# Optimization experiments

Measured on AMD Instinct MI355X. Metric: run time of the kernel, lower is better.

The kernel has to match this reference:

```python
import jax, jax.numpy as jnp
import numpy as np

EMBED_DIM = 1024
NUM_HEADS = 16
HEAD_DIM = EMBED_DIM // NUM_HEADS
ROPE_BASE = 10000.0


def setup_inputs() -> dict:
    key = jax.random.key(0)
    ks = jax.random.split(key, 5)
    B, S, E = 4, 2048, EMBED_DIM
    hidden = jax.random.normal(ks[0], (B, S, E), dtype=jnp.float32)
    sc_in = 1.0 / np.sqrt(E)
    qkv_w = jax.random.normal(ks[1], (3 * E, E), dtype=jnp.float32) * sc_in
    qkv_b = jnp.zeros((3 * E,), dtype=jnp.float32)
    proj_w = jax.random.normal(ks[2], (E, E), dtype=jnp.float32) * sc_in
    proj_b = jnp.zeros((E,), dtype=jnp.float32)
    return {"hidden": hidden, "qkv_w": qkv_w, "qkv_b": qkv_b,
            "proj_w": proj_w, "proj_b": proj_b}


def _rope_cos_sin(position_ids, head_dim, base):
    # position_ids: [B, S] int; returns cos/sin of shape [B, 1, S, head_dim]
    inv_freq = 1.0 / (base ** (jnp.arange(0, head_dim, 2, dtype=jnp.float32) / head_dim))
    freqs = position_ids.astype(jnp.float32)[..., None] * inv_freq  # [B,S,hd/2]
    emb = jnp.concatenate([freqs, freqs], axis=-1)                  # [B,S,hd]
    return jnp.cos(emb)[:, None], jnp.sin(emb)[:, None]


def _rotate_half(x):
    x1, x2 = jnp.split(x, 2, axis=-1)
    return jnp.concatenate([-x2, x1], axis=-1)


def reference(hidden, qkv_w, qkv_b, proj_w, proj_b):
    B, S, E = hidden.shape
    H, hd = NUM_HEADS, HEAD_DIM
    qkv = hidden @ qkv_w.T + qkv_b                    # [B,S,3E]
    qkv = qkv.reshape(B, S, 3, H, hd).transpose(2, 0, 3, 1, 4)  # [3,B,H,S,hd]
    q, k, v = qkv[0], qkv[1], qkv[2]
    pos = jnp.broadcast_to(jnp.arange(S)[None, :], (B, S))
    cos, sin = _rope_cos_sin(pos, hd, ROPE_BASE)      # [B,1,S,hd]
    q = q * cos + _rotate_half(q) * sin
    k = k * cos + _rotate_half(k) * sin
    scale = 1.0 / jnp.sqrt(jnp.float32(hd))
    scores = jnp.einsum("bhsd,bhtd->bhst", q, k) * scale
    attn = jax.nn.softmax(scores, axis=-1)
    out = jnp.einsum("bhst,bhtd->bhsd", attn, v)      # [B,H,S,hd]
    out = out.transpose(0, 2, 1, 3).reshape(B, S, E)
    return out @ proj_w.T + proj_b
```

## Files before the change

kernel.cpp:

```cpp
#include <hip/hip_runtime.h>
#include <cstdint>
#include <cstddef>

typedef _Float16 f16;
typedef __attribute__((ext_vector_type(4))) float f32x4;
typedef __attribute__((ext_vector_type(8))) _Float16 f16x8;
typedef __attribute__((ext_vector_type(4))) _Float16 f16x4;

#define S_SEQ 2048
#define E_DIM 1024

#define OFF_HID   0ull
#define OFF_QKVW  8388608ull
#define OFF_PROJW 11534336ull
#define OFF_Q     12582912ull
#define OFF_K     20971520ull
#define OFF_VT    29360128ull
#define OFF_AO    37748736ull

__device__ __forceinline__ void async_copy16(const void* g, void* l) {
  __builtin_amdgcn_global_load_lds(
      (const __attribute__((address_space(1))) unsigned int*)g,
      (__attribute__((address_space(3))) unsigned int*)l, 16, 0, 0);
}

__device__ __forceinline__ float fast_exp2(float x) {
#if __has_builtin(__builtin_amdgcn_exp2f)
  return __builtin_amdgcn_exp2f(x);
#else
  return __expf(x * 0.6931471805599453f);
#endif
}

__global__ __launch_bounds__(256) void cvt_kernel(const float* __restrict__ hid,
                                                  const float* __restrict__ qw,
                                                  const float* __restrict__ pw,
                                                  f16* __restrict__ ws) {
  long i = (long)blockIdx.x * 256 + threadIdx.x;
  const float* src;
  f16* dst;
  long idx;
  if (i < 2097152L) { src = hid; dst = ws + OFF_HID;  idx = i; }
  else if (i < 2883584L) { src = qw; dst = ws + OFF_QKVW; idx = i - 2097152L; }
  else { src = pw; dst = ws + OFF_PROJW; idx = i - 2883584L; }
  float4 v = *(const float4*)(src + idx * 4);
  f16x4 o = { (f16)v.x, (f16)v.y, (f16)v.z, (f16)v.w };
  *(f16x4*)(dst + idx * 4) = o;
}

template <int MODE>
__global__ __launch_bounds__(256)
void gemm_kernel(const f16* __restrict__ A, const f16* __restrict__ Bm,
                 const float* __restrict__ bias,
                 f16* __restrict__ q_out, f16* __restrict__ k_out,
                 f16* __restrict__ vT_out, float* __restrict__ f_out) {
  __shared__ __align__(16) f16 As[2][128 * 32];
  __shared__ __align__(16) f16 Bs[2][128 * 32];
  const int tid = threadIdx.x;
  const int wave = tid >> 6;
  const int lane = tid & 63;
  const int q4 = lane >> 4;
  const int l16 = lane & 15;
  const int m0 = blockIdx.y * 128;
  const int n0 = blockIdx.x * 128;
  const int wr = (wave >> 1) * 64;
  const int wc = (wave & 1) * 64;
  f32x4 acc[4][4] = {};

  const int srow = tid >> 2;
  const int scol = (tid & 3) * 8;

  auto stage = [&](int k0, int b) {
    for (int p = 0; p < 2; ++p) {
      int row = p * 64 + srow;
      async_copy16(A + (size_t)(m0 + row) * 1024 + k0 + scol,
                   &As[b][(size_t)(p * 256 + wave * 64) * 8]);
      async_copy16(Bm + (size_t)(n0 + row) * 1024 + k0 + scol,
                   &Bs[b][(size_t)(p * 256 + wave * 64) * 8]);
    }
  };

  stage(0, 0);
  __syncthreads();
  int buf = 0;
  for (int k0 = 0; k0 < 1024; k0 += 32) {
    if (k0 + 32 < 1024) stage(k0 + 32, buf ^ 1);
    f16x8 af[4], bf[4];
    for (int mt = 0; mt < 4; ++mt)
      af[mt] = *(const f16x8*)&As[buf][(wr + mt * 16 + l16) * 32 + q4 * 8];
    for (int nt = 0; nt < 4; ++nt)
      bf[nt] = *(const f16x8*)&Bs[buf][(wc + nt * 16 + l16) * 32 + q4 * 8];
    for (int mt = 0; mt < 4; ++mt)
      for (int nt = 0; nt < 4; ++nt)
        acc[mt][nt] = __builtin_amdgcn_mfma_f32_16x16x32_f16(af[mt], bf[nt],
                                                             acc[mt][nt], 0, 0, 0);
    __syncthreads();
    buf ^= 1;
  }

  if constexpr (MODE == 0) {
    const int bx = blockIdx.x;
    const int part = bx >> 3;
    const int h = (((bx & 7) * 128) + wc) >> 6;
    float bv[4];
    for (int nt = 0; nt < 4; ++nt) bv[nt] = bias[n0 + wc + nt * 16 + l16];
    if (part < 2) {
      f16* outp = (part == 0) ? q_out : k_out;
      const float qscale = (part == 0) ? 0.18033688011112042f : 1.0f;
      float invf[2];
      for (int nt = 0; nt < 2; ++nt)
        invf[nt] = __expf(-(float)(nt * 16 + l16) * 0.2878231366242557f);
      for (int mt = 0; mt < 4; ++mt) {
        int mbase = m0 + wr + mt * 16 + q4 * 4;
        for (int r = 0; r < 4; ++r) {
          int mm = mbase + r;
          int b = mm >> 11, s = mm & 2047;
          size_t rowb = ((size_t)((b * 16 + h) * 2048 + s)) * 64;
          for (int nt = 0; nt < 2; ++nt) {
            float x1 = acc[mt][nt][r] + bv[nt];
            float x2 = acc[mt][nt + 2][r] + bv[nt + 2];
            float ang = (float)s * invf[nt];
            float sn, cs;
            __sincosf(ang, &sn, &cs);
            float o1 = (x1 * cs - x2 * sn) * qscale;
            float o2 = (x2 * cs + x1 * sn) * qscale;
            int d1 = nt * 16 + l16;
            outp[rowb + d1] = (f16)o1;
            outp[rowb + d1 + 32] = (f16)o2;
          }
        }
      }
    } else {
      for (int mt = 0; mt < 4; ++mt) {
        int mbase = m0 + wr + mt * 16 + q4 * 4;
        int b = mbase >> 11, s0 = mbase & 2047;
        for (int nt = 0; nt < 4; ++nt) {
          int d = nt * 16 + l16;
          size_t basei = ((size_t)((b * 16 + h) * 64 + d)) * 2048 + s0;
          f16x4 pk;
          for (int r = 0; r < 4; ++r) pk[r] = (f16)(acc[mt][nt][r] + bv[nt]);
          *(f16x4*)&vT_out[basei] = pk;
        }
      }
    }
  } else {
    float bv[4];
    for (int nt = 0; nt < 4; ++nt) bv[nt] = bias[n0 + wc + nt * 16 + l16];
    for (int mt = 0; mt < 4; ++mt)
      for (int r = 0; r < 4; ++r) {
        int mm = m0 + wr + mt * 16 + q4 * 4 + r;
        for (int nt = 0; nt < 4; ++nt)
          f_out[(size_t)mm * 1024 + n0 + wc + nt * 16 + l16] = acc[mt][nt][r] + bv[nt];
      }
  }
}

__global__ __launch_bounds__(256, 4)
void attn_kernel(const f16* __restrict__ Qg, const f16* __restrict__ Kg,
                 const f16* __restrict__ VTg, f16* __restrict__ AOg) {
  __shared__ __align__(16) f16 smem[2][2 * 64 * 72];
  const int tid = threadIdx.x;
  const int wave = tid >> 6, lane = tid & 63;
  const int q4 = lane >> 4, l16 = lane & 15;
  const int qt = blockIdx.x, bh = blockIdx.y;
  const f16* Qb = Qg + (size_t)bh * (S_SEQ * 64);
  const f16* Kb = Kg + (size_t)bh * (S_SEQ * 64);
  const f16* Vb = VTg + (size_t)bh * (64 * S_SEQ);
  const int ws0 = wave * 32;

  f16x8 qf[2][2];
  for (int sn = 0; sn < 2; ++sn)
    for (int kf = 0; kf < 2; ++kf)
      qf[sn][kf] = *(const f16x8*)(Qb + (size_t)(qt * 128 + ws0 + sn * 16 + l16) * 64
                                      + kf * 32 + q4 * 8);

  f32x4 o[4][2] = {};
  float lsum[2] = {0.f, 0.f};

  const int srow = tid >> 3;
  const int scol = (tid & 7) * 8;

  int4 k0r = *(const int4*)(Kb + (size_t)srow * 64 + scol);
  int4 k1r = *(const int4*)(Kb + (size_t)(32 + srow) * 64 + scol);
  int4 v0r = *(const int4*)(Vb + (size_t)srow * 2048 + scol);
  int4 v1r = *(const int4*)(Vb + (size_t)(32 + srow) * 2048 + scol);
  {
    f16* Kn = smem[0];
    f16* Vn = smem[0] + 64 * 72;
    *(int4*)(Kn + srow * 72 + scol) = k0r;
    *(int4*)(Kn + (32 + srow) * 72 + scol) = k1r;
    *(int4*)(Vn + srow * 72 + scol) = v0r;
    *(int4*)(Vn + (32 + srow) * 72 + scol) = v1r;
  }
  __syncthreads();

  int cur = 0;
  for (int tt = 0; tt < 32; ++tt) {
    const f16* Kc = smem[cur];
    const f16* Vc = smem[cur] + 64 * 72;

    if (tt + 1 < 32) {
      const int t0n = (tt + 1) * 64;
      k0r = *(const int4*)(Kb + (size_t)(t0n + srow) * 64 + scol);
      k1r = *(const int4*)(Kb + (size_t)(t0n + 32 + srow) * 64 + scol);
      v0r = *(const int4*)(Vb + (size_t)srow * 2048 + t0n + scol);
      v1r = *(const int4*)(Vb + (size_t)(32 + srow) * 2048 + t0n + scol);
    }

    f32x4 st[4][2];
    for (int tm = 0; tm < 4; ++tm) {
      f16x8 k0 = *(const f16x8*)(Kc + (tm * 16 + l16) * 72 + q4 * 8);
      f16x8 k1 = *(const f16x8*)(Kc + (tm * 16 + l16) * 72 + 32 + q4 * 8);
      for (int sn = 0; sn < 2; ++sn) {
        f32x4 c = {0.f, 0.f, 0.f, 0.f};
        c = __builtin_amdgcn_mfma_f32_16x16x32_f16(k0, qf[sn][0], c, 0, 0, 0);
        c = __builtin_amdgcn_mfma_f32_16x16x32_f16(k1, qf[sn][1], c, 0, 0, 0);
        st[tm][sn] = c;
      }
    }

    for (int sn = 0; sn < 2; ++sn) {
      float rs = 0.f;
      for (int tm = 0; tm < 4; ++tm)
        for (int r = 0; r < 4; ++r) {
          float p = fast_exp2(st[tm][sn][r]);
          st[tm][sn][r] = p;
          rs += p;
        }
      lsum[sn] += rs;
    }

    for (int tm = 0; tm < 4; ++tm) {
      f16x4 vfr[4];
      for (int dm = 0; dm < 4; ++dm)
        vfr[dm] = *(const f16x4*)(Vc + (dm * 16 + l16) * 72 + tm * 16 + q4 * 4);
      for (int sn = 0; sn < 2; ++sn) {
        f16x4 pfr;
        pfr[0] = (f16)st[tm][sn][0];
        pfr[1] = (f16)st[tm][sn][1];
        pfr[2] = (f16)st[tm][sn][2];
        pfr[3] = (f16)st[tm][sn][3];
        for (int dm = 0; dm < 4; ++dm)
          o[dm][sn] = __builtin_amdgcn_mfma_f32_16x16x16f16(vfr[dm], pfr,
                                                            o[dm][sn], 0, 0, 0);
      }
    }

    if (tt + 1 < 32) {
      f16* Kn = smem[cur ^ 1];
      f16* Vn = smem[cur ^ 1] + 64 * 72;
      *(int4*)(Kn + srow * 72 + scol) = k0r;
      *(int4*)(Kn + (32 + srow) * 72 + scol) = k1r;
      *(int4*)(Vn + srow * 72 + scol) = v0r;
      *(int4*)(Vn + (32 + srow) * 72 + scol) = v1r;
    }
    __syncthreads();
    cur ^= 1;
  }

  float inv_l[2];
  for (int sn = 0; sn < 2; ++sn) {
    float l = lsum[sn];
    l += __shfl_xor(l, 16, 64);
    l += __shfl_xor(l, 32, 64);
    inv_l[sn] = 1.0f / l;
  }
  f16* Ot = smem[0];
  for (int sn = 0; sn < 2; ++sn) {
    int so = ws0 + sn * 16 + l16;
    for (int dm = 0; dm < 4; ++dm) {
      f16x4 w;
      w[0] = (f16)(o[dm][sn][0] * inv_l[sn]);
      w[1] = (f16)(o[dm][sn][1] * inv_l[sn]);
      w[2] = (f16)(o[dm][sn][2] * inv_l[sn]);
      w[3] = (f16)(o[dm][sn][3] * inv_l[sn]);
      *(f16x4*)(Ot + so * 72 + dm * 16 + q4 * 4) = w;
    }
  }
  __syncthreads();
  const int b = bh >> 4, h = bh & 15;
  const int sr = tid >> 1, dh = (tid & 1) * 32;
  size_t gbase = ((size_t)(b * 2048 + qt * 128 + sr)) * 1024 + h * 64 + dh;
  for (int c = 0; c < 4; ++c) {
    f16x8 v = *(const f16x8*)(Ot + sr * 72 + dh + c * 8);
    *(f16x8*)(AOg + gbase + c * 8) = v;
  }
}

extern "C" void kernel_launch(void* const* d_in, const int* in_sizes, int n_in,
                              void* d_out, int out_size, void* d_ws, size_t ws_size,
                              hipStream_t stream) {
  const float* hid   = (const float*)d_in[0];
  const float* qkvw  = (const float*)d_in[1];
  const float* qkvb  = (const float*)d_in[2];
  const float* projw = (const float*)d_in[3];
  const float* projb = (const float*)d_in[4];
  float* out = (float*)d_out;
  f16* ws = (f16*)d_ws;

  cvt_kernel<<<12288, 256, 0, stream>>>(hid, qkvw, projw, ws);
  gemm_kernel<0><<<dim3(24, 64), 256, 0, stream>>>(
      ws + OFF_HID, ws + OFF_QKVW, qkvb,
      ws + OFF_Q, ws + OFF_K, ws + OFF_VT, nullptr);
  attn_kernel<<<dim3(16, 64), 256, 0, stream>>>(
      ws + OFF_Q, ws + OFF_K, ws + OFF_VT, ws + OFF_AO);
  gemm_kernel<1><<<dim3(8, 64), 256, 0, stream>>>(
      ws + OFF_AO, ws + OFF_PROJW, projb,
      nullptr, nullptr, nullptr, out);
}
```

Measured before the change: 283.3 us.

## Enlarge attention query tile to 256 rows, swizzle V layout, use MFMA row sums

```diff
diff --git a/kernel.cpp b/kernel.cpp
--- a/kernel.cpp
+++ b/kernel.cpp
@@ -155,10 +155,10 @@
   }
 }
 
-__global__ __launch_bounds__(256, 4)
+__global__ __launch_bounds__(256, 2)
 void attn_kernel(const f16* __restrict__ Qg, const f16* __restrict__ Kg,
                  const f16* __restrict__ VTg, f16* __restrict__ AOg) {
-  __shared__ __align__(16) f16 smem[2][2 * 64 * 72];
+  __shared__ __align__(16) f16 smem[2][8704];
   const int tid = threadIdx.x;
   const int wave = tid >> 6, lane = tid & 63;
   const int q4 = lane >> 4, l16 = lane & 15;
@@ -166,124 +166,159 @@
   const f16* Qb = Qg + (size_t)bh * (S_SEQ * 64);
   const f16* Kb = Kg + (size_t)bh * (S_SEQ * 64);
   const f16* Vb = VTg + (size_t)bh * (64 * S_SEQ);
-  const int ws0 = wave * 32;
-
-  f16x8 qf[2][2];
-  for (int sn = 0; sn < 2; ++sn)
+  const int ws0 = wave * 64;
+
+  f16x8 qf[4][2];
+#pragma unroll
+  for (int sn = 0; sn < 4; ++sn)
+#pragma unroll
     for (int kf = 0; kf < 2; ++kf)
-      qf[sn][kf] = *(const f16x8*)(Qb + (size_t)(qt * 128 + ws0 + sn * 16 + l16) * 64
+      qf[sn][kf] = *(const f16x8*)(Qb + (size_t)(qt * 256 + ws0 + sn * 16 + l16) * 64
                                       + kf * 32 + q4 * 8);
 
-  f32x4 o[4][2] = {};
-  float lsum[2] = {0.f, 0.f};
+  f32x4 o[4][4] = {};
+  f32x4 lacc[4] = {};
+  f16x8 ones;
+#pragma unroll
+  for (int j = 0; j < 8; ++j) ones[j] = (f16)1.0f;
 
   const int srow = tid >> 3;
   const int scol = (tid & 7) * 8;
 
+  const int kcs = scol >> 5;
+  const int hs8 = ((scol >> 4) & 1) * 8;
+  const int q0s = (scol & 15) >> 2;
+  const int slot0 = kcs * 4 + q0s;
+  const int swzA = (((slot0) ^ (srow & 7)) << 4) + hs8;
+  const int swzB = (((slot0 + 1) ^ (srow & 7)) << 4) + hs8;
+
   int4 k0r = *(const int4*)(Kb + (size_t)srow * 64 + scol);
   int4 k1r = *(const int4*)(Kb + (size_t)(32 + srow) * 64 + scol);
-  int4 v0r = *(const int4*)(Vb + (size_t)srow * 2048 + scol);
-  int4 v1r = *(const int4*)(Vb + (size_t)(32 + srow) * 2048 + scol);
+  f16x8 v0r = *(const f16x8*)(Vb + (size_t)srow * 2048 + scol);
+  f16x8 v1r = *(const f16x8*)(Vb + (size_t)(32 + srow) * 2048 + scol);
   {
     f16* Kn = smem[0];
-    f16* Vn = smem[0] + 64 * 72;
+    char* Vn = (char*)(smem[0] + 4608);
     *(int4*)(Kn + srow * 72 + scol) = k0r;
     *(int4*)(Kn + (32 + srow) * 72 + scol) = k1r;
-    *(int4*)(Vn + srow * 72 + scol) = v0r;
-    *(int4*)(Vn + (32 + srow) * 72 + scol) = v1r;
+    f16x4 lo0 = {v0r[0], v0r[1], v0r[2], v0r[3]};
+    f16x4 hi0 = {v0r[4], v0r[5], v0r[6], v0r[7]};
+    f16x4 lo1 = {v1r[0], v1r[1], v1r[2], v1r[3]};
+    f16x4 hi1 = {v1r[4], v1r[5], v1r[6], v1r[7]};
+    *(f16x4*)(Vn + srow * 128 + swzA) = lo0;
+    *(f16x4*)(Vn + srow * 128 + swzB) = hi0;
+    *(f16x4*)(Vn + (32 + srow) * 128 + swzA) = lo1;
+    *(f16x4*)(Vn + (32 + srow) * 128 + swzB) = hi1;
   }
   __syncthreads();
 
   int cur = 0;
   for (int tt = 0; tt < 32; ++tt) {
     const f16* Kc = smem[cur];
-    const f16* Vc = smem[cur] + 64 * 72;
+    const char* Vc = (const char*)(smem[cur] + 4608);
 
     if (tt + 1 < 32) {
       const int t0n = (tt + 1) * 64;
       k0r = *(const int4*)(Kb + (size_t)(t0n + srow) * 64 + scol);
       k1r = *(const int4*)(Kb + (size_t)(t0n + 32 + srow) * 64 + scol);
-      v0r = *(const int4*)(Vb + (size_t)srow * 2048 + t0n + scol);
-      v1r = *(const int4*)(Vb + (size_t)(32 + srow) * 2048 + t0n + scol);
-    }
-
-    f32x4 st[4][2];
+      v0r = *(const f16x8*)(Vb + (size_t)srow * 2048 + t0n + scol);
+      v1r = *(const f16x8*)(Vb + (size_t)(32 + srow) * 2048 + t0n + scol);
+    }
+
+    f16x8 kf0[4], kf1[4];
+#pragma unroll
     for (int tm = 0; tm < 4; ++tm) {
-      f16x8 k0 = *(const f16x8*)(Kc + (tm * 16 + l16) * 72 + q4 * 8);
-      f16x8 k1 = *(const f16x8*)(Kc + (tm * 16 + l16) * 72 + 32 + q4 * 8);
-      for (int sn = 0; sn < 2; ++sn) {
+      kf0[tm] = *(const f16x8*)(Kc + (tm * 16 + l16) * 72 + q4 * 8);
+      kf1[tm] = *(const f16x8*)(Kc + (tm * 16 + l16) * 72 + 32 + q4 * 8);
+    }
+    f16x8 vf[4][2];
+#pragma unroll
+    for (int dm = 0; dm < 4; ++dm)
+#pragma unroll
+      for (int kc = 0; kc < 2; ++kc)
+        vf[dm][kc] = *(const f16x8*)(Vc + (dm * 16 + l16) * 128 +
+                                     (((kc * 4 + q4) ^ (l16 & 7)) << 4));
+
+#pragma unroll
+    for (int sn = 0; sn < 4; ++sn) {
+      f32x4 st[4];
+#pragma unroll
+      for (int tm = 0; tm < 4; ++tm) {
         f32x4 c = {0.f, 0.f, 0.f, 0.f};
-        c = __builtin_amdgcn_mfma_f32_16x16x32_f16(k0, qf[sn][0], c, 0, 0, 0);
-        c = __builtin_amdgcn_mfma_f32_16x16x32_f16(k1, qf[sn][1], c, 0, 0, 0);
-        st[tm][sn] = c;
-      }
-    }
-
-    for (int sn = 0; sn < 2; ++sn) {
-      float rs = 0.f;
+        c = __builtin_amdgcn_mfma_f32_16x16x32_f16(kf0[tm], qf[sn][0], c, 0, 0, 0);
+        c = __builtin_amdgcn_mfma_f32_16x16x32_f16(kf1[tm], qf[sn][1], c, 0, 0, 0);
+        st[tm] = c;
+      }
+#pragma unroll
       for (int tm = 0; tm < 4; ++tm)
-        for (int r = 0; r < 4; ++r) {
-          float p = fast_exp2(st[tm][sn][r]);
-          st[tm][sn][r] = p;
-          rs += p;
-        }
-      lsum[sn] += rs;
-    }
-
-    for (int tm = 0; tm < 4; ++tm) {
-      f16x4 vfr[4];
-      for (int dm = 0; dm < 4; ++dm)
-        vfr[dm] = *(const f16x4*)(Vc + (dm * 16 + l16) * 72 + tm * 16 + q4 * 4);
-      for (int sn = 0; sn < 2; ++sn) {
-        f16x4 pfr;
-        pfr[0] = (f16)st[tm][sn][0];
-        pfr[1] = (f16)st[tm][sn][1];
-        pfr[2] = (f16)st[tm][sn][2];
-        pfr[3] = (f16)st[tm][sn][3];
+#pragma unroll
+        for (int r = 0; r < 4; ++r)
+          st[tm][r] = fast_exp2(st[tm][r]);
+#pragma unroll
+      for (int kc = 0; kc < 2; ++kc) {
+        f16x8 pf;
+        pf[0] = (f16)st[kc * 2][0];
+        pf[1] = (f16)st[kc * 2][1];
+        pf[2] = (f16)st[kc * 2][2];
+        pf[3] = (f16)st[kc * 2][3];
+        pf[4] = (f16)st[kc * 2 + 1][0];
+        pf[5] = (f16)st[kc * 2 + 1][1];
+        pf[6] = (f16)st[kc * 2 + 1][2];
+        pf[7] = (f16)st[kc * 2 + 1][3];
+        lacc[sn] = __builtin_amdgcn_mfma_f32_16x16x32_f16(ones, pf, lacc[sn], 0, 0, 0);
+#pragma unroll
         for (int dm = 0; dm < 4; ++dm)
-          o[dm][sn] = __builtin_amdgcn_mfma_f32_16x16x16f16(vfr[dm], pfr,
-                                                            o[dm][sn], 0, 0, 0);
+          o[dm][sn] = __builtin_amdgcn_mfma_f32_16x16x32_f16(vf[dm][kc], pf,
+                                                             o[dm][sn], 0, 0, 0);
       }
     }
 
     if (tt + 1 < 32) {
       f16* Kn = smem[cur ^ 1];
-      f16* Vn = smem[cur ^ 1] + 64 * 72;
+      char* Vn = (char*)(smem[cur ^ 1] + 4608);
       *(int4*)(Kn + srow * 72 + scol) = k0r;
       *(int4*)(Kn + (32 + srow) * 72 + scol) = k1r;
-      *(int4*)(Vn + srow * 72 + scol) = v0r;
-      *(int4*)(Vn + (32 + srow) * 72 + scol) = v1r;
+      f16x4 lo0 = {v0r[0], v0r[1], v0r[2], v0r[3]};
+      f16x4 hi0 = {v0r[4], v0r[5], v0r[6], v0r[7]};
+      f16x4 lo1 = {v1r[0], v1r[1], v1r[2], v1r[3]};
+      f16x4 hi1 = {v1r[4], v1r[5], v1r[6], v1r[7]};
+      *(f16x4*)(Vn + srow * 128 + swzA) = lo0;
+      *(f16x4*)(Vn + srow * 128 + swzB) = hi0;
+      *(f16x4*)(Vn + (32 + srow) * 128 + swzA) = lo1;
+      *(f16x4*)(Vn + (32 + srow) * 128 + swzB) = hi1;
     }
     __syncthreads();
     cur ^= 1;
   }
 
-  float inv_l[2];
-  for (int sn = 0; sn < 2; ++sn) {
-    float l = lsum[sn];
-    l += __shfl_xor(l, 16, 64);
-    l += __shfl_xor(l, 32, 64);
-    inv_l[sn] = 1.0f / l;
-  }
+  float inv_l[4];
+#pragma unroll
+  for (int sn = 0; sn < 4; ++sn) inv_l[sn] = 1.0f / lacc[sn][0];
   f16* Ot = smem[0];
-  for (int sn = 0; sn < 2; ++sn) {
+#pragma unroll
+  for (int sn = 0; sn < 4; ++sn) {
     int so = ws0 + sn * 16 + l16;
+#pragma unroll
     for (int dm = 0; dm < 4; ++dm) {
       f16x4 w;
       w[0] = (f16)(o[dm][sn][0] * inv_l[sn]);
       w[1] = (f16)(o[dm][sn][1] * inv_l[sn]);
       w[2] = (f16)(o[dm][sn][2] * inv_l[sn]);
       w[3] = (f16)(o[dm][sn][3] * inv_l[sn]);
-      *(f16x4*)(Ot + so * 72 + dm * 16 + q4 * 4) = w;
+      *(f16x4*)(Ot + so * 64 + dm * 16 + q4 * 4) = w;
     }
   }
   __syncthreads();
   const int b = bh >> 4, h = bh & 15;
-  const int sr = tid >> 1, dh = (tid & 1) * 32;
-  size_t gbase = ((size_t)(b * 2048 + qt * 128 + sr)) * 1024 + h * 64 + dh;
-  for (int c = 0; c < 4; ++c) {
-    f16x8 v = *(const f16x8*)(Ot + sr * 72 + dh + c * 8);
-    *(f16x8*)(AOg + gbase + c * 8) = v;
+#pragma unroll
+  for (int half = 0; half < 2; ++half) {
+    const int sr = half * 128 + (tid >> 1), dh = (tid & 1) * 32;
+    size_t gbase = ((size_t)(b * 2048 + qt * 256 + sr)) * 1024 + h * 64 + dh;
+#pragma unroll
+    for (int c = 0; c < 4; ++c) {
+      f16x8 v = *(const f16x8*)(Ot + sr * 64 + dh + c * 8);
+      *(f16x8*)(AOg + gbase + c * 8) = v;
+    }
   }
 }
 
@@ -302,7 +337,7 @@
   gemm_kernel<0><<<dim3(24, 64), 256, 0, stream>>>(
       ws + OFF_HID, ws + OFF_QKVW, qkvb,
       ws + OFF_Q, ws + OFF_K, ws + OFF_VT, nullptr);
-  attn_kernel<<<dim3(16, 64), 256, 0, stream>>>(
+  attn_kernel<<<dim3(8, 64), 256, 0, stream>>>(
       ws + OFF_Q, ws + OFF_K, ws + OFF_VT, ws + OFF_AO);
   gemm_kernel<1><<<dim3(8, 64), 256, 0, stream>>>(
       ws + OFF_AO, ws + OFF_PROJW, projb,
```

Measured after the change: 269.0 us. -5.1%, faster.
